# Performance work log

Hardware: AMD Instinct MI355X
Metric: run time of the kernel (lower is better)

Reference implementation:

```python
import jax, jax.numpy as jnp
import numpy as np

EPS = 1e-5
BS, NA, NC, NL, NPTS, ED, NG = 1, 900, 6, 4, 13, 256, 8
GD = ED // NG
IMG_W, IMG_H = 704.0, 256.0
FMAP_HW = [(64, 176), (32, 88), (16, 44), (8, 22)]


def _ln(x, g, b):
    m = x.mean(-1, keepdims=True)
    v = ((x - m) ** 2).mean(-1, keepdims=True)
    return (x - m) / jnp.sqrt(v + EPS) * g + b


def _grid_sample(img, grid):
    # img: [N,C,H,W]; grid: [N,P,Q,2] in [-1,1]; bilinear, zeros padding, align_corners=False
    N, C, H, W = img.shape
    gx = jnp.clip((grid[..., 0] + 1.0) * (W * 0.5) - 0.5, -1e4, 1e4)
    gy = jnp.clip((grid[..., 1] + 1.0) * (H * 0.5) - 0.5, -1e4, 1e4)
    x0 = jnp.floor(gx); y0 = jnp.floor(gy)
    wx1 = gx - x0; wy1 = gy - y0; wx0 = 1.0 - wx1; wy0 = 1.0 - wy1
    x0i = x0.astype(jnp.int32); y0i = y0.astype(jnp.int32)
    flat = img.reshape(N, C, H * W)

    def corner(xi, yi, wgt):
        valid = (xi >= 0) & (xi < W) & (yi >= 0) & (yi < H)
        idx = (jnp.clip(yi, 0, H - 1) * W + jnp.clip(xi, 0, W - 1))
        g = jax.vmap(lambda f, i: f[:, i])(flat, idx.reshape(N, -1))  # [N,C,P*Q]
        g = g.reshape(N, C, idx.shape[1], idx.shape[2])
        return g * (wgt * valid)[:, None]

    return (corner(x0i, y0i, wx0 * wy0) + corner(x0i + 1, y0i, wx1 * wy0)
            + corner(x0i, y0i + 1, wx0 * wy1) + corner(x0i + 1, y0i + 1, wx1 * wy1))


def setup_inputs() -> dict:
    key = jax.random.key(0)
    ks = jax.random.split(key, 20)
    d = {}
    d['instance_feature'] = jax.random.normal(ks[0], (BS, NA, ED), jnp.float32)
    xyz = jax.random.normal(ks[1], (BS, NA, 3), jnp.float32) * 1.5
    size = jax.random.normal(ks[2], (BS, NA, 3), jnp.float32) * 0.3
    theta = jax.random.uniform(ks[3], (BS, NA, 1), jnp.float32) * (2.0 * np.pi)
    vel = jax.random.normal(ks[4], (BS, NA, 3), jnp.float32) * 0.1
    d['anchor'] = jnp.concatenate([xyz, size, jnp.sin(theta), jnp.cos(theta), vel], -1)
    d['anchor_embed'] = jax.random.normal(ks[5], (BS, NA, ED), jnp.float32)
    for i, (h, w) in enumerate(FMAP_HW):
        d[f'fmap{i}'] = jax.random.normal(ks[6 + i], (BS, NC, ED, h, w), jnp.float32)
    base = jnp.array([[80., 0., 0., 352.], [0., 80., 0., 128.],
                      [0., 0., 0., 1.], [0., 0., 0., 1.]], jnp.float32)
    proj = jnp.tile(base, (BS, NC, 1, 1))
    proj = proj.at[:, :, :2, :].add(jax.random.normal(ks[10], (BS, NC, 2, 4), jnp.float32) * 2.0)
    d['projection_mat'] = proj
    d['image_wh'] = jnp.broadcast_to(jnp.array([IMG_W, IMG_H], jnp.float32), (BS, NC, 2))
    d['fix_scale'] = jnp.array([[0, 0, 0], [0.45, 0, 0], [-0.45, 0, 0], [0, 0.45, 0],
                                [0, -0.45, 0], [0, 0, 0.45], [0, 0, -0.45]], jnp.float32)

    def w(k, shape):
        return jax.random.normal(k, shape, jnp.float32) * 0.02

    d['lfc_w'] = w(ks[11], (ED, 6 * 3)); d['lfc_b'] = jnp.zeros((18,), jnp.float32)
    d['cam_w1'] = w(ks[12], (12, ED)); d['cam_b1'] = jnp.zeros((ED,), jnp.float32)
    d['cam_g1'] = jnp.ones((ED,), jnp.float32); d['cam_be1'] = jnp.zeros((ED,), jnp.float32)
    d['cam_w2'] = w(ks[13], (ED, ED)); d['cam_b2'] = jnp.zeros((ED,), jnp.float32)
    d['cam_g2'] = jnp.ones((ED,), jnp.float32); d['cam_be2'] = jnp.zeros((ED,), jnp.float32)
    d['wfc_w'] = w(ks[14], (ED, NG * NL * NPTS)); d['wfc_b'] = jnp.zeros((NG * NL * NPTS,), jnp.float32)
    d['op_w'] = w(ks[15], (ED, ED)); d['op_b'] = jnp.zeros((ED,), jnp.float32)
    return d


def reference(instance_feature, anchor, anchor_embed, fmap0, fmap1, fmap2, fmap3,
              projection_mat, image_wh, fix_scale, lfc_w, lfc_b,
              cam_w1, cam_b1, cam_g1, cam_be1, cam_w2, cam_b2, cam_g2, cam_be2,
              wfc_w, wfc_b, op_w, op_b):
    bs, na = instance_feature.shape[:2]
    # ---- keypoint generation ----
    size = jnp.exp(anchor[..., None, 3:6])                       # [bs,na,1,3]
    kp = fix_scale * size                                        # [bs,na,7,3]
    ls = jax.nn.sigmoid(instance_feature @ lfc_w + lfc_b).reshape(bs, na, -1, 3) - 0.5
    kp = jnp.concatenate([kp, ls * size], axis=-2)               # [bs,na,NPTS,3]
    sin, cos = anchor[..., 6:7], anchor[..., 7:8]                # [bs,na,1]
    kx, ky, kz = kp[..., 0], kp[..., 1], kp[..., 2]
    key_points = jnp.stack([cos * kx - sin * ky, sin * kx + cos * ky, kz], -1) \
                 + anchor[..., None, 0:3]                        # [bs,na,NPTS,3]
    # ---- per-cam/level/point group weights ----
    feat = instance_feature + anchor_embed
    cam_in = projection_mat[:, :, :3].reshape(bs, NC, 12)
    h = jax.nn.relu(cam_in @ cam_w1 + cam_b1); h = _ln(h, cam_g1, cam_be1)
    h = jax.nn.relu(h @ cam_w2 + cam_b2); cam_embed = _ln(h, cam_g2, cam_be2)
    f = feat[:, :, None] + cam_embed[:, None]                    # [bs,na,NC,ED]
    wts = (f @ wfc_w + wfc_b).reshape(bs, na, NC * NL * NPTS, NG)
    wts = jax.nn.softmax(wts, axis=-2).reshape(bs, na, NC, NL, NPTS, NG)
    # ---- multi-cam projection + bilinear sampling ----
    pts = jnp.concatenate([key_points, jnp.ones_like(key_points[..., :1])], -1)
    p2d = jnp.einsum('bcij,banj->bcani', projection_mat, pts)    # [bs,NC,na,NPTS,4]
    p2d = p2d[..., :2] / jnp.maximum(p2d[..., 2:3], 1e-5)
    p2d = p2d / image_wh[:, :, None, None]
    grid = (p2d * 2.0 - 1.0).reshape(bs * NC, na, NPTS, 2)
    feats = jnp.stack([_grid_sample(fm.reshape(bs * NC, ED, fm.shape[-2], fm.shape[-1]), grid)
                       for fm in (fmap0, fmap1, fmap2, fmap3)], axis=1)  # [bs*NC,NL,ED,na,NPTS]
    feats = feats.reshape(bs, NC, NL, ED, na, NPTS).transpose(0, 4, 1, 2, 5, 3)  # [bs,na,NC,NL,NPTS,ED]
    # ---- group-weighted fusion over cams & levels, then sum over points ----
    fg = feats.reshape(bs, na, NC, NL, NPTS, NG, GD)
    fused = jnp.einsum('bnclpg,bnclpgd->bnpgd', wts, fg).reshape(bs, na, NPTS, ED)
    fused = fused.sum(axis=2)                                    # [bs,na,ED]
    out = fused @ op_w + op_b
    return jnp.concatenate([out, instance_feature], axis=-1)     # [bs,na,2*ED]
```

## Files before the change

### kernel.cpp

```cpp
#include <hip/hip_runtime.h>
#include <stdint.h>

#define NA 900
#define NC 6
#define NL 4
#define NPTS 13
#define ED 256
#define NG 8
#define LNEPS 1e-5f
#define NSTAGE 718303
#define NSTAGE_BLOCKS 2806
#define NTRANS 5616
#define NCOPY 672
#define NSAMP 312

struct PIn { const void* p[24]; };

__device__ __forceinline__ float b2f(unsigned short u){
  union { uint32_t i; float f; } v; v.i = ((uint32_t)u)<<16; return v.f;
}
__device__ __forceinline__ unsigned short f2b(float f){
  union { float f; uint32_t i; } v; v.f = f;
  uint32_t r = v.i + 0x7FFFu + ((v.i>>16)&1u);
  return (unsigned short)(r>>16);
}
#define BLO(u) __uint_as_float((u)<<16)
#define BHI(u) __uint_as_float((u)&0xffff0000u)

__device__ __forceinline__ float ldx(const void* p, int i, bool bf){
  return bf ? b2f(((const unsigned short*)p)[i]) : ((const float*)p)[i];
}

__device__ __forceinline__ bool sniff_bf(const unsigned short* __restrict__ u16){
  int lane = threadIdx.x & 63;
  unsigned short u = u16[2*lane];
  int e = (u>>7)&0xFF;
  int sane = (e>=110 && e<=135) ? 1 : 0;
  #pragma unroll
  for (int m=32;m;m>>=1) sane += __shfl_xor(sane, m);
  return sane >= 48;
}

__device__ __forceinline__ void blockReduce2(float& a, float& b, float* lds){
  #pragma unroll
  for (int m=32;m;m>>=1){ a += __shfl_xor(a,m); b += __shfl_xor(b,m); }
  int w = threadIdx.x>>6;
  if ((threadIdx.x&63)==0){ lds[w]=a; lds[w+4]=b; }
  __syncthreads();
  a = lds[0]+lds[1]+lds[2]+lds[3];
  b = lds[4]+lds[5]+lds[6]+lds[7];
  __syncthreads();
}

__global__ __launch_bounds__(256) void k_prep(PIn in, float* __restrict__ stage,
                                              unsigned short* __restrict__ tf,
                                              unsigned short* __restrict__ wfcw_h,
                                              unsigned short* __restrict__ opw_h,
                                              float* __restrict__ Bc){
  const bool bf = sniff_bf((const unsigned short*)in.p[0]);
  const int tid = threadIdx.x;
  int b = blockIdx.x;

  __shared__ unsigned short T[64][68];
  __shared__ float h[ED];
  __shared__ float cE[ED];
  __shared__ float red8[8];
  __shared__ float part[4][64];

  if (b < NSTAGE_BLOCKS){
    const int cum[21] = {0,230400,240300,470700,470796,470808,470829,475437,475455,
                         478527,478783,479039,479295,544831,545087,545343,545599,
                         652095,652511,718047,718303};
    const int map[20] = {0,1,2,7,8,9,10,11,12,13,14,15,16,17,18,19,20,21,22,23};
    int idx = b*256 + tid;
    if (idx >= NSTAGE) return;
    int seg = 0, base = 0;
    #pragma unroll
    for (int s=1;s<20;s++) if (idx >= cum[s]){ seg = s; base = cum[s]; }
    const void* src = in.p[map[0]];
    #pragma unroll
    for (int s=1;s<20;s++) if (seg==s) src = in.p[map[s]];
    stage[idx] = ldx(src, idx - base, bf);
    return;
  }
  b -= NSTAGE_BLOCKS;
  if (b < NTRANS){
    const int xb[4]  = {176,44,11,3};
    const int HWs[4] = {11264,2816,704,176};
    const int TFO[4] = {0,17301504,21626880,22708224};
    int l, local;
    if      (b < 4224){ l=0; local=b;      }
    else if (b < 5280){ l=1; local=b-4224; }
    else if (b < 5544){ l=2; local=b-5280; }
    else              { l=3; local=b-5544; }
    int pt = local % xb[l]; int rest = local / xb[l];
    int ct = rest & 3; int c = rest >> 2;
    const int HW = HWs[l];
    const int px0 = pt*64;
    const void* src = in.p[3+l];
    #pragma unroll
    for (int p=0;p<2;p++){
      int lch = p*32 + (tid>>3);
      int gch = ct*64 + lch;
      int pxv = (tid&7)*8;
      size_t base = (size_t)(c*ED+gch)*HW + px0 + pxv;
      unsigned short v[8];
      if (px0 + pxv + 8 <= HW){
        if (bf){
          uint4 q = *reinterpret_cast<const uint4*>((const unsigned short*)src + base);
          v[0]=q.x&0xffff; v[1]=q.x>>16; v[2]=q.y&0xffff; v[3]=q.y>>16;
          v[4]=q.z&0xffff; v[5]=q.z>>16; v[6]=q.w&0xffff; v[7]=q.w>>16;
        } else {
          float4 f0 = *reinterpret_cast<const float4*>((const float*)src + base);
          float4 f1 = *reinterpret_cast<const float4*>((const float*)src + base + 4);
          v[0]=f2b(f0.x); v[1]=f2b(f0.y); v[2]=f2b(f0.z); v[3]=f2b(f0.w);
          v[4]=f2b(f1.x); v[5]=f2b(f1.y); v[6]=f2b(f1.z); v[7]=f2b(f1.w);
        }
      } else {
        #pragma unroll
        for (int i=0;i<8;i++){
          int px = px0+pxv+i;
          v[i] = (px<HW) ? (bf ? ((const unsigned short*)src)[base+i]
                               : f2b(((const float*)src)[base+i])) : (unsigned short)0;
        }
      }
      #pragma unroll
      for (int i=0;i<8;i++) T[pxv+i][lch] = v[i];
    }
    __syncthreads();
    unsigned short* dst = tf + TFO[l] + (size_t)c*HW*ED + ct*64;
    #pragma unroll
    for (int p=0;p<2;p++){
      int pxl = p*32 + (tid>>3);
      int px = px0 + pxl;
      if (px >= HW) continue;
      int ch8 = (tid&7)*8;
      ushort4 lo = *reinterpret_cast<ushort4*>(&T[pxl][ch8]);
      ushort4 hi = *reinterpret_cast<ushort4*>(&T[pxl][ch8+4]);
      union { ushort4 hh[2]; uint4 q; } u;
      u.hh[0]=lo; u.hh[1]=hi;
      *reinterpret_cast<uint4*>(dst + (size_t)px*ED + ch8) = u.q;
    }
    return;
  }
  b -= NTRANS;
  if (b < NCOPY){
    int idx = b*256 + tid;
    if (idx < 106496){
      wfcw_h[idx] = bf ? ((const unsigned short*)in.p[20])[idx]
                       : f2b(((const float*)in.p[20])[idx]);
    } else {
      int j = idx - 106496;
      opw_h[j] = bf ? ((const unsigned short*)in.p[22])[j]
                    : f2b(((const float*)in.p[22])[j]);
    }
    return;
  }
  b -= NCOPY;
  {
    const void* proj = in.p[7];
    const void* w1 = in.p[12]; const void* b1 = in.p[13];
    const void* g1 = in.p[14]; const void* be1 = in.p[15];
    const void* w2 = in.p[16]; const void* b2 = in.p[17];
    const void* g2 = in.p[18]; const void* be2 = in.p[19];
    const void* wfcw = in.p[20]; const void* wfcb = in.p[21];
    const int c = b/7, colt = b - (b/7)*7;
    float ci[12];
    #pragma unroll
    for (int i=0;i<12;i++) ci[i] = ldx(proj, c*16+i, bf);
    float acc = ldx(b1, tid, bf);
    #pragma unroll
    for (int k=0;k<12;k++) acc += ci[k]*ldx(w1, k*ED+tid, bf);
    float x = fmaxf(acc, 0.f);
    float s=x, q=x*x;
    blockReduce2(s,q,red8);
    float mean = s*(1.f/ED), var = q*(1.f/ED)-mean*mean;
    h[tid] = (x-mean)*rsqrtf(var+LNEPS)*ldx(g1,tid,bf) + ldx(be1,tid,bf);
    __syncthreads();
    acc = ldx(b2, tid, bf);
    #pragma unroll 8
    for (int k=0;k<ED;k++) acc += h[k]*ldx(w2, k*ED+tid, bf);
    x = fmaxf(acc,0.f);
    s=x; q=x*x;
    blockReduce2(s,q,red8);
    mean = s*(1.f/ED); var = q*(1.f/ED)-mean*mean;
    cE[tid] = (x-mean)*rsqrtf(var+LNEPS)*ldx(g2,tid,bf) + ldx(be2,tid,bf);
    __syncthreads();
    const int kc = tid>>6, colL = tid&63, col = colt*64+colL;
    float a = 0.f;
    if (col < 416){
      #pragma unroll 8
      for (int k=0;k<64;k++) a += cE[kc*64+k]*ldx(wfcw, (kc*64+k)*416+col, bf);
    }
    part[kc][colL] = a;
    __syncthreads();
    if (kc==0 && col<416)
      Bc[c*416+col] = part[0][colL]+part[1][colL]+part[2][colL]+part[3][colL] + ldx(wfcb,col,bf);
  }
}

__global__ __launch_bounds__(256) void k_anchor(
    const float* __restrict__ stage, const unsigned short* __restrict__ tf,
    const unsigned short* __restrict__ wfcw_h, const unsigned short* __restrict__ opw_h,
    const float* __restrict__ Bc, const void* __restrict__ rawinst,
    void* __restrict__ outv){
  const int n = blockIdx.x, tid = threadIdx.x;
  const bool bf = sniff_bf((const unsigned short*)rawinst);

  const float* s_inst = stage + 0;
  const float* s_anc  = stage + 230400;
  const float* s_ae   = stage + 240300;
  const float* s_proj = stage + 470700;
  const float* s_imwh = stage + 470796;
  const float* s_fixs = stage + 470808;
  const float* s_lw   = stage + 470829;
  const float* s_lb   = stage + 475437;
  const float* s_opb  = stage + 718047;

  __shared__ float ifs[ED];
  __shared__ float fe[ED];
  __shared__ float lg[NC*416];
  __shared__ uint4 cbi[NSAMP];
  __shared__ uint4 cwf[NSAMP];
  __shared__ unsigned short coff[NSAMP];
  __shared__ float red[8][ED+4];
  __shared__ float fu[ED];
  __shared__ float kp[13][3];
  __shared__ float sc[8];
  __shared__ float lsv[18];
  __shared__ int scnt;

  {
    if (tid==0) scnt = 0;
    float iv = s_inst[n*ED+tid];
    ifs[tid] = iv;
    fe[tid]  = iv + s_ae[n*ED+tid];
    if (tid < 3)       sc[tid] = s_anc[n*11+tid];
    else if (tid == 3) sc[3]   = s_anc[n*11+6];
    else if (tid == 4) sc[4]   = s_anc[n*11+7];
    else if (tid < 8)  sc[tid] = __expf(s_anc[n*11+tid-2]);
  }
  __syncthreads();
  if (tid < 144){
    int d = tid>>3, j = tid&7;
    float a = 0.f;
    #pragma unroll 8
    for (int k=j*32;k<j*32+32;k++) a += ifs[k]*s_lw[k*18+d];
    a += __shfl_xor(a,1); a += __shfl_xor(a,2); a += __shfl_xor(a,4);
    if (j==0){
      a += s_lb[d];
      lsv[d] = 1.f/(1.f+__expf(-a)) - 0.5f;
    }
  }
  __syncthreads();
  if (tid < 13){
    float kx,ky,kz;
    if (tid < 7){
      kx = s_fixs[tid*3+0]*sc[5];
      ky = s_fixs[tid*3+1]*sc[6];
      kz = s_fixs[tid*3+2]*sc[7];
    } else {
      int j = tid-7;
      kx = lsv[j*3+0]*sc[5]; ky = lsv[j*3+1]*sc[6]; kz = lsv[j*3+2]*sc[7];
    }
    kp[tid][0] = sc[4]*kx - sc[3]*ky + sc[0];
    kp[tid][1] = sc[3]*kx + sc[4]*ky + sc[1];
    kp[tid][2] = kz + sc[2];
  }
  {
    int col2 = (tid < 160) ? tid+256 : 415;
    float a0 = 0.f, a1 = 0.f;
    #pragma unroll 4
    for (int k=0;k<ED;k++){
      float fv = fe[k];
      a0 += fv*b2f(wfcw_h[k*416+tid]);
      a1 += fv*b2f(wfcw_h[k*416+col2]);
    }
    #pragma unroll
    for (int c=0;c<NC;c++){
      lg[c*416+tid] = a0 + Bc[c*416+tid];
      if (tid < 160) lg[c*416+tid+256] = a1 + Bc[c*416+tid+256];
    }
  }
  __syncthreads();
  #pragma unroll
  for (int pass=0;pass<2;pass++){
    int s = tid + pass*256;
    if (s < NSAMP){
      int c = s/52, rr = s - c*52;
      int l = rr/13, p = rr - l*13;
      float m[12];
      #pragma unroll
      for (int i=0;i<12;i++) m[i] = s_proj[c*16+i];
      float X=kp[p][0], Y=kp[p][1], Z=kp[p][2];
      float x = m[0]*X + m[1]*Y + m[2]*Z  + m[3];
      float y = m[4]*X + m[5]*Y + m[6]*Z  + m[7];
      float z = m[8]*X + m[9]*Y + m[10]*Z + m[11];
      float d = fmaxf(z, 1e-5f);
      float px = x/(d*s_imwh[c*2+0]), py = y/(d*s_imwh[c*2+1]);
      const int W = 176>>l, H = 64>>l;
      const int TFO[4] = {0,17301504,21626880,22708224};
      float gx = fminf(fmaxf(px*(float)W - 0.5f, -10000.f), 10000.f);
      float gy = fminf(fmaxf(py*(float)H - 0.5f, -10000.f), 10000.f);
      float xf = floorf(gx), yf = floorf(gy);
      int x0 = (int)xf, y0 = (int)yf;
      float wx1 = gx-xf, wy1 = gy-yf;
      float wx0 = 1.f-wx1, wy0 = 1.f-wy1;
      bool vx0 = (x0>=0)&&(x0<W),   vx1 = (x0+1>=0)&&(x0+1<W);
      bool vy0 = (y0>=0)&&(y0<H),   vy1 = (y0+1>=0)&&(y0+1<H);
      float w00 = (vx0&&vy0) ? wx0*wy0 : 0.f;
      float w10 = (vx1&&vy0) ? wx1*wy0 : 0.f;
      float w01 = (vx0&&vy1) ? wx0*wy1 : 0.f;
      float w11 = (vx1&&vy1) ? wx1*wy1 : 0.f;
      if (w00+w10+w01+w11 != 0.f){
        int cx0 = min(max(x0,0),W-1), cx1 = min(max(x0+1,0),W-1);
        int cy0 = min(max(y0,0),H-1), cy1 = min(max(y0+1,0),H-1);
        uint32_t cam = (uint32_t)TFO[l] + (uint32_t)(c*H*W)*ED;
        uint4 bi, wv;
        bi.x = cam + (uint32_t)(cy0*W+cx0)*ED;
        bi.y = cam + (uint32_t)(cy0*W+cx1)*ED;
        bi.z = cam + (uint32_t)(cy1*W+cx0)*ED;
        bi.w = cam + (uint32_t)(cy1*W+cx1)*ED;
        wv.x = __float_as_uint(w00); wv.y = __float_as_uint(w10);
        wv.z = __float_as_uint(w01); wv.w = __float_as_uint(w11);
        int slot = atomicAdd(&scnt, 1);
        cbi[slot] = bi;
        cwf[slot] = wv;
        coff[slot] = (unsigned short)(c*416 + rr*8);
      }
    }
  }
  {
    const int g = tid>>5, j = tid&31;
    float v[10]; float m = -1e30f;
    #pragma unroll
    for (int i=0;i<10;i++){
      int e = j + 32*i;
      float val = -1e30f;
      if (e < NSAMP){
        int c = e/52, rr = e - c*52;
        val = lg[c*416 + rr*8 + g];
        m = fmaxf(m, val);
      }
      v[i] = val;
    }
    #pragma unroll
    for (int mk=16;mk;mk>>=1) m = fmaxf(m, __shfl_xor(m, mk, 32));
    float sum = 0.f;
    #pragma unroll
    for (int i=0;i<10;i++){
      if (j + 32*i < NSAMP){ float ex = __expf(v[i]-m); v[i] = ex; sum += ex; }
    }
    #pragma unroll
    for (int mk=16;mk;mk>>=1) sum += __shfl_xor(sum, mk, 32);
    float inv = 1.f/sum;
    #pragma unroll
    for (int i=0;i<10;i++){
      int e = j + 32*i;
      if (e < NSAMP){
        int c = e/52, rr = e - c*52;
        lg[c*416 + rr*8 + g] = v[i]*inv;
      }
    }
  }
  __syncthreads();
  {
    const int m = scnt;
    const int strm = tid>>5, lane32 = tid&31;
    const int ch8 = lane32*8, gg = lane32>>2;
    float acc[8] = {0,0,0,0,0,0,0,0};
    int i = strm;
    for (; i + 8 < m; i += 16){
      uint4 biA = cbi[i],   wfA = cwf[i];
      uint4 biB = cbi[i+8], wfB = cwf[i+8];
      float wgA = lg[coff[i]+gg],  wgB = lg[coff[i+8]+gg];
      uint4 a00 = *reinterpret_cast<const uint4*>(tf + biA.x + ch8);
      uint4 a10 = *reinterpret_cast<const uint4*>(tf + biA.y + ch8);
      uint4 a01 = *reinterpret_cast<const uint4*>(tf + biA.z + ch8);
      uint4 a11 = *reinterpret_cast<const uint4*>(tf + biA.w + ch8);
      uint4 b00 = *reinterpret_cast<const uint4*>(tf + biB.x + ch8);
      uint4 b10 = *reinterpret_cast<const uint4*>(tf + biB.y + ch8);
      uint4 b01 = *reinterpret_cast<const uint4*>(tf + biB.z + ch8);
      uint4 b11 = *reinterpret_cast<const uint4*>(tf + biB.w + ch8);
      float pA00 = wgA*__uint_as_float(wfA.x), pA10 = wgA*__uint_as_float(wfA.y);
      float pA01 = wgA*__uint_as_float(wfA.z), pA11 = wgA*__uint_as_float(wfA.w);
      float pB00 = wgB*__uint_as_float(wfB.x), pB10 = wgB*__uint_as_float(wfB.y);
      float pB01 = wgB*__uint_as_float(wfB.z), pB11 = wgB*__uint_as_float(wfB.w);
      acc[0] += pA00*BLO(a00.x)+pA10*BLO(a10.x)+pA01*BLO(a01.x)+pA11*BLO(a11.x)
              + pB00*BLO(b00.x)+pB10*BLO(b10.x)+pB01*BLO(b01.x)+pB11*BLO(b11.x);
      acc[1] += pA00*BHI(a00.x)+pA10*BHI(a10.x)+pA01*BHI(a01.x)+pA11*BHI(a11.x)
              + pB00*BHI(b00.x)+pB10*BHI(b10.x)+pB01*BHI(b01.x)+pB11*BHI(b11.x);
      acc[2] += pA00*BLO(a00.y)+pA10*BLO(a10.y)+pA01*BLO(a01.y)+pA11*BLO(a11.y)
              + pB00*BLO(b00.y)+pB10*BLO(b10.y)+pB01*BLO(b01.y)+pB11*BLO(b11.y);
      acc[3] += pA00*BHI(a00.y)+pA10*BHI(a10.y)+pA01*BHI(a01.y)+pA11*BHI(a11.y)
              + pB00*BHI(b00.y)+pB10*BHI(b10.y)+pB01*BHI(b01.y)+pB11*BHI(b11.y);
      acc[4] += pA00*BLO(a00.z)+pA10*BLO(a10.z)+pA01*BLO(a01.z)+pA11*BLO(a11.z)
              + pB00*BLO(b00.z)+pB10*BLO(b10.z)+pB01*BLO(b01.z)+pB11*BLO(b11.z);
      acc[5] += pA00*BHI(a00.z)+pA10*BHI(a10.z)+pA01*BHI(a01.z)+pA11*BHI(a11.z)
              + pB00*BHI(b00.z)+pB10*BHI(b10.z)+pB01*BHI(b01.z)+pB11*BHI(b11.z);
      acc[6] += pA00*BLO(a00.w)+pA10*BLO(a10.w)+pA01*BLO(a01.w)+pA11*BLO(a11.w)
              + pB00*BLO(b00.w)+pB10*BLO(b10.w)+pB01*BLO(b01.w)+pB11*BLO(b11.w);
      acc[7] += pA00*BHI(a00.w)+pA10*BHI(a10.w)+pA01*BHI(a01.w)+pA11*BHI(a11.w)
              + pB00*BHI(b00.w)+pB10*BHI(b10.w)+pB01*BHI(b01.w)+pB11*BHI(b11.w);
    }
    for (; i < m; i += 8){
      uint4 bi = cbi[i], wf = cwf[i];
      float wg = lg[coff[i]+gg];
      uint4 q00 = *reinterpret_cast<const uint4*>(tf + bi.x + ch8);
      uint4 q10 = *reinterpret_cast<const uint4*>(tf + bi.y + ch8);
      uint4 q01 = *reinterpret_cast<const uint4*>(tf + bi.z + ch8);
      uint4 q11 = *reinterpret_cast<const uint4*>(tf + bi.w + ch8);
      float p00 = wg*__uint_as_float(wf.x), p10 = wg*__uint_as_float(wf.y);
      float p01 = wg*__uint_as_float(wf.z), p11 = wg*__uint_as_float(wf.w);
      acc[0] += p00*BLO(q00.x)+p10*BLO(q10.x)+p01*BLO(q01.x)+p11*BLO(q11.x);
      acc[1] += p00*BHI(q00.x)+p10*BHI(q10.x)+p01*BHI(q01.x)+p11*BHI(q11.x);
      acc[2] += p00*BLO(q00.y)+p10*BLO(q10.y)+p01*BLO(q01.y)+p11*BLO(q11.y);
      acc[3] += p00*BHI(q00.y)+p10*BHI(q10.y)+p01*BHI(q01.y)+p11*BHI(q11.y);
      acc[4] += p00*BLO(q00.z)+p10*BLO(q10.z)+p01*BLO(q01.z)+p11*BLO(q11.z);
      acc[5] += p00*BHI(q00.z)+p10*BHI(q10.z)+p01*BHI(q01.z)+p11*BHI(q11.z);
      acc[6] += p00*BLO(q00.w)+p10*BLO(q10.w)+p01*BLO(q01.w)+p11*BLO(q11.w);
      acc[7] += p00*BHI(q00.w)+p10*BHI(q10.w)+p01*BHI(q01.w)+p11*BHI(q11.w);
    }
    *reinterpret_cast<float4*>(&red[strm][ch8])   = make_float4(acc[0],acc[1],acc[2],acc[3]);
    *reinterpret_cast<float4*>(&red[strm][ch8+4]) = make_float4(acc[4],acc[5],acc[6],acc[7]);
  }
  __syncthreads();
  {
    float r = 0.f;
    #pragma unroll
    for (int i=0;i<8;i++) r += red[i][tid];
    fu[tid] = r;
  }
  __syncthreads();
  {
    float acc = s_opb[tid];
    #pragma unroll 4
    for (int k=0;k<ED;k++) acc += fu[k]*b2f(opw_h[k*ED+tid]);
    float pv = ifs[tid];
    if (bf){
      unsigned short* outh = (unsigned short*)outv;
      outh[n*512+tid]     = f2b(acc);
      outh[n*512+256+tid] = f2b(pv);
    } else {
      float* outf = (float*)outv;
      outf[n*512+tid]     = acc;
      outf[n*512+256+tid] = pv;
    }
  }
}

extern "C" void kernel_launch(void* const* d_in, const int* in_sizes, int n_in,
                              void* d_out, int out_size, void* d_ws, size_t ws_size,
                              hipStream_t stream){
  char* ws = (char*)d_ws;
  size_t off = 0;
  auto alloc = [&](size_t bytes)->char*{
    char* p = ws + off; off += (bytes + 63) & ~size_t(63); return p;
  };
  unsigned short* tf = (unsigned short*)alloc((size_t)22978560*2);
  float* stage  = (float*)alloc((size_t)NSTAGE*4);
  unsigned short* wfcw_h = (unsigned short*)alloc((size_t)106496*2);
  unsigned short* opw_h  = (unsigned short*)alloc((size_t)65536*2);
  float* Bc     = (float*)alloc((size_t)NC*416*4);

  PIn in;
  for (int i=0;i<24;i++) in.p[i] = d_in[i];

  k_prep<<<NSTAGE_BLOCKS + NTRANS + NCOPY + 42, 256, 0, stream>>>(in, stage, tf, wfcw_h, opw_h, Bc);
  k_anchor<<<NA, 256, 0, stream>>>(stage, tf, wfcw_h, opw_h, Bc, d_in[0], d_out);
}
```

Before: 255.8 us.

## Double k_anchor block to 512 threads and relayout softmax logits per group

Launches the per-anchor kernel with 512 threads instead of 256. The extra threads split the logit GEMV (one column per thread), the sample projection (a single pass), the gather streams (16 instead of 8) and the output projection (split-K over two halves). Logits are stored group-major with a padded stride, so the softmax reads them contiguously with full 64-lane wavefronts. This raises per-anchor parallelism and latency hiding in exchange for more threads per block, larger shared memory for the reduction buffer, and extra barriers.

```diff
diff --git a/kernel.cpp b/kernel.cpp
--- a/kernel.cpp
+++ b/kernel.cpp
@@ -13,6 +13,7 @@
 #define NTRANS 5616
 #define NCOPY 672
 #define NSAMP 312
+#define LGS 313
 
 struct PIn { const void* p[24]; };
 
@@ -199,7 +200,7 @@
   }
 }
 
-__global__ __launch_bounds__(256) void k_anchor(
+__global__ __launch_bounds__(512, 8) void k_anchor(
     const float* __restrict__ stage, const unsigned short* __restrict__ tf,
     const unsigned short* __restrict__ wfcw_h, const unsigned short* __restrict__ opw_h,
     const float* __restrict__ Bc, const void* __restrict__ rawinst,
@@ -219,26 +220,28 @@
 
   __shared__ float ifs[ED];
   __shared__ float fe[ED];
-  __shared__ float lg[NC*416];
+  __shared__ float lg2[8*LGS];
   __shared__ uint4 cbi[NSAMP];
   __shared__ uint4 cwf[NSAMP];
   __shared__ unsigned short coff[NSAMP];
-  __shared__ float red[8][ED+4];
+  __shared__ float red[16][ED+4];
   __shared__ float fu[ED];
   __shared__ float kp[13][3];
   __shared__ float sc[8];
   __shared__ float lsv[18];
   __shared__ int scnt;
 
-  {
-    if (tid==0) scnt = 0;
+  if (tid < 256){
     float iv = s_inst[n*ED+tid];
     ifs[tid] = iv;
     fe[tid]  = iv + s_ae[n*ED+tid];
-    if (tid < 3)       sc[tid] = s_anc[n*11+tid];
-    else if (tid == 3) sc[3]   = s_anc[n*11+6];
-    else if (tid == 4) sc[4]   = s_anc[n*11+7];
-    else if (tid < 8)  sc[tid] = __expf(s_anc[n*11+tid-2]);
+  } else {
+    int t = tid - 256;
+    if (t == 0)      scnt = 0;
+    if (t < 3)       sc[t] = s_anc[n*11+t];
+    else if (t == 3) sc[3] = s_anc[n*11+6];
+    else if (t == 4) sc[4] = s_anc[n*11+7];
+    else if (t < 8)  sc[t] = __expf(s_anc[n*11+t-2]);
   }
   __syncthreads();
   if (tid < 144){
@@ -267,100 +270,87 @@
     kp[tid][1] = sc[3]*kx + sc[4]*ky + sc[1];
     kp[tid][2] = kz + sc[2];
   }
+  if (tid < 416){
+    float a0 = 0.f;
+    #pragma unroll 8
+    for (int k=0;k<ED;k++) a0 += fe[k]*b2f(wfcw_h[k*416+tid]);
+    const int g = tid & 7, rr = tid >> 3;
+    #pragma unroll
+    for (int c=0;c<NC;c++)
+      lg2[g*LGS + c*52 + rr] = a0 + Bc[c*416+tid];
+  }
+  __syncthreads();
+  if (tid < NSAMP){
+    int s = tid;
+    int c = s/52, rr = s - c*52;
+    int l = rr/13, p = rr - l*13;
+    float m[12];
+    #pragma unroll
+    for (int i=0;i<12;i++) m[i] = s_proj[c*16+i];
+    float X=kp[p][0], Y=kp[p][1], Z=kp[p][2];
+    float x = m[0]*X + m[1]*Y + m[2]*Z  + m[3];
+    float y = m[4]*X + m[5]*Y + m[6]*Z  + m[7];
+    float z = m[8]*X + m[9]*Y + m[10]*Z + m[11];
+    float d = fmaxf(z, 1e-5f);
+    float px = x/(d*s_imwh[c*2+0]), py = y/(d*s_imwh[c*2+1]);
+    const int W = 176>>l, H = 64>>l;
+    const int TFO[4] = {0,17301504,21626880,22708224};
+    float gx = fminf(fmaxf(px*(float)W - 0.5f, -10000.f), 10000.f);
+    float gy = fminf(fmaxf(py*(float)H - 0.5f, -10000.f), 10000.f);
+    float xf = floorf(gx), yf = floorf(gy);
+    int x0 = (int)xf, y0 = (int)yf;
+    float wx1 = gx-xf, wy1 = gy-yf;
+    float wx0 = 1.f-wx1, wy0 = 1.f-wy1;
+    bool vx0 = (x0>=0)&&(x0<W),   vx1 = (x0+1>=0)&&(x0+1<W);
+    bool vy0 = (y0>=0)&&(y0<H),   vy1 = (y0+1>=0)&&(y0+1<H);
+    float w00 = (vx0&&vy0) ? wx0*wy0 : 0.f;
+    float w10 = (vx1&&vy0) ? wx1*wy0 : 0.f;
+    float w01 = (vx0&&vy1) ? wx0*wy1 : 0.f;
+    float w11 = (vx1&&vy1) ? wx1*wy1 : 0.f;
+    if (w00+w10+w01+w11 != 0.f){
+      int cx0 = min(max(x0,0),W-1), cx1 = min(max(x0+1,0),W-1);
+      int cy0 = min(max(y0,0),H-1), cy1 = min(max(y0+1,0),H-1);
+      uint32_t cam = (uint32_t)TFO[l] + (uint32_t)(c*H*W)*ED;
+      uint4 bi, wv;
+      bi.x = cam + (uint32_t)(cy0*W+cx0)*ED;
+      bi.y = cam + (uint32_t)(cy0*W+cx1)*ED;
+      bi.z = cam + (uint32_t)(cy1*W+cx0)*ED;
+      bi.w = cam + (uint32_t)(cy1*W+cx1)*ED;
+      wv.x = __float_as_uint(w00); wv.y = __float_as_uint(w10);
+      wv.z = __float_as_uint(w01); wv.w = __float_as_uint(w11);
+      int slot = atomicAdd(&scnt, 1);
+      cbi[slot] = bi;
+      cwf[slot] = wv;
+      coff[slot] = (unsigned short)s;
+    }
+  }
   {
-    int col2 = (tid < 160) ? tid+256 : 415;
-    float a0 = 0.f, a1 = 0.f;
-    #pragma unroll 4
-    for (int k=0;k<ED;k++){
-      float fv = fe[k];
-      a0 += fv*b2f(wfcw_h[k*416+tid]);
-      a1 += fv*b2f(wfcw_h[k*416+col2]);
-    }
-    #pragma unroll
-    for (int c=0;c<NC;c++){
-      lg[c*416+tid] = a0 + Bc[c*416+tid];
-      if (tid < 160) lg[c*416+tid+256] = a1 + Bc[c*416+tid+256];
-    }
-  }
-  __syncthreads();
-  #pragma unroll
-  for (int pass=0;pass<2;pass++){
-    int s = tid + pass*256;
-    if (s < NSAMP){
-      int c = s/52, rr = s - c*52;
-      int l = rr/13, p = rr - l*13;
-      float m[12];
-      #pragma unroll
-      for (int i=0;i<12;i++) m[i] = s_proj[c*16+i];
-      float X=kp[p][0], Y=kp[p][1], Z=kp[p][2];
-      float x = m[0]*X + m[1]*Y + m[2]*Z  + m[3];
-      float y = m[4]*X + m[5]*Y + m[6]*Z  + m[7];
-      float z = m[8]*X + m[9]*Y + m[10]*Z + m[11];
-      float d = fmaxf(z, 1e-5f);
-      float px = x/(d*s_imwh[c*2+0]), py = y/(d*s_imwh[c*2+1]);
-      const int W = 176>>l, H = 64>>l;
-      const int TFO[4] = {0,17301504,21626880,22708224};
-      float gx = fminf(fmaxf(px*(float)W - 0.5f, -10000.f), 10000.f);
-      float gy = fminf(fmaxf(py*(float)H - 0.5f, -10000.f), 10000.f);
-      float xf = floorf(gx), yf = floorf(gy);
-      int x0 = (int)xf, y0 = (int)yf;
-      float wx1 = gx-xf, wy1 = gy-yf;
-      float wx0 = 1.f-wx1, wy0 = 1.f-wy1;
-      bool vx0 = (x0>=0)&&(x0<W),   vx1 = (x0+1>=0)&&(x0+1<W);
-      bool vy0 = (y0>=0)&&(y0<H),   vy1 = (y0+1>=0)&&(y0+1<H);
-      float w00 = (vx0&&vy0) ? wx0*wy0 : 0.f;
-      float w10 = (vx1&&vy0) ? wx1*wy0 : 0.f;
-      float w01 = (vx0&&vy1) ? wx0*wy1 : 0.f;
-      float w11 = (vx1&&vy1) ? wx1*wy1 : 0.f;
-      if (w00+w10+w01+w11 != 0.f){
-        int cx0 = min(max(x0,0),W-1), cx1 = min(max(x0+1,0),W-1);
-        int cy0 = min(max(y0,0),H-1), cy1 = min(max(y0+1,0),H-1);
-        uint32_t cam = (uint32_t)TFO[l] + (uint32_t)(c*H*W)*ED;
-        uint4 bi, wv;
-        bi.x = cam + (uint32_t)(cy0*W+cx0)*ED;
-        bi.y = cam + (uint32_t)(cy0*W+cx1)*ED;
-        bi.z = cam + (uint32_t)(cy1*W+cx0)*ED;
-        bi.w = cam + (uint32_t)(cy1*W+cx1)*ED;
-        wv.x = __float_as_uint(w00); wv.y = __float_as_uint(w10);
-        wv.z = __float_as_uint(w01); wv.w = __float_as_uint(w11);
-        int slot = atomicAdd(&scnt, 1);
-        cbi[slot] = bi;
-        cwf[slot] = wv;
-        coff[slot] = (unsigned short)(c*416 + rr*8);
-      }
-    }
-  }
-  {
-    const int g = tid>>5, j = tid&31;
-    float v[10]; float m = -1e30f;
-    #pragma unroll
-    for (int i=0;i<10;i++){
-      int e = j + 32*i;
+    const int g = tid>>6, j = tid&63;
+    float v[5]; float mx = -1e30f;
+    #pragma unroll
+    for (int i=0;i<5;i++){
+      int e = j + 64*i;
       float val = -1e30f;
       if (e < NSAMP){
-        int c = e/52, rr = e - c*52;
-        val = lg[c*416 + rr*8 + g];
-        m = fmaxf(m, val);
+        val = lg2[g*LGS + e];
+        mx = fmaxf(mx, val);
       }
       v[i] = val;
     }
     #pragma unroll
-    for (int mk=16;mk;mk>>=1) m = fmaxf(m, __shfl_xor(m, mk, 32));
+    for (int mk=32;mk;mk>>=1) mx = fmaxf(mx, __shfl_xor(mx, mk));
     float sum = 0.f;
     #pragma unroll
-    for (int i=0;i<10;i++){
-      if (j + 32*i < NSAMP){ float ex = __expf(v[i]-m); v[i] = ex; sum += ex; }
-    }
-    #pragma unroll
-    for (int mk=16;mk;mk>>=1) sum += __shfl_xor(sum, mk, 32);
+    for (int i=0;i<5;i++){
+      if (j + 64*i < NSAMP){ float ex = __expf(v[i]-mx); v[i] = ex; sum += ex; }
+    }
+    #pragma unroll
+    for (int mk=32;mk;mk>>=1) sum += __shfl_xor(sum, mk);
     float inv = 1.f/sum;
     #pragma unroll
-    for (int i=0;i<10;i++){
-      int e = j + 32*i;
-      if (e < NSAMP){
-        int c = e/52, rr = e - c*52;
-        lg[c*416 + rr*8 + g] = v[i]*inv;
-      }
+    for (int i=0;i<5;i++){
+      int e = j + 64*i;
+      if (e < NSAMP) lg2[g*LGS + e] = v[i]*inv;
     }
   }
   __syncthreads();
@@ -370,10 +360,10 @@
     const int ch8 = lane32*8, gg = lane32>>2;
     float acc[8] = {0,0,0,0,0,0,0,0};
     int i = strm;
-    for (; i + 8 < m; i += 16){
-      uint4 biA = cbi[i],   wfA = cwf[i];
-      uint4 biB = cbi[i+8], wfB = cwf[i+8];
-      float wgA = lg[coff[i]+gg],  wgB = lg[coff[i+8]+gg];
+    for (; i + 16 < m; i += 32){
+      uint4 biA = cbi[i],    wfA = cwf[i];
+      uint4 biB = cbi[i+16], wfB = cwf[i+16];
+      float wgA = lg2[gg*LGS + coff[i]],  wgB = lg2[gg*LGS + coff[i+16]];
       uint4 a00 = *reinterpret_cast<const uint4*>(tf + biA.x + ch8);
       uint4 a10 = *reinterpret_cast<const uint4*>(tf + biA.y + ch8);
       uint4 a01 = *reinterpret_cast<const uint4*>(tf + biA.z + ch8);
@@ -403,9 +393,9 @@
       acc[7] += pA00*BHI(a00.w)+pA10*BHI(a10.w)+pA01*BHI(a01.w)+pA11*BHI(a11.w)
               + pB00*BHI(b00.w)+pB10*BHI(b10.w)+pB01*BHI(b01.w)+pB11*BHI(b11.w);
     }
-    for (; i < m; i += 8){
+    for (; i < m; i += 16){
       uint4 bi = cbi[i], wf = cwf[i];
-      float wg = lg[coff[i]+gg];
+      float wg = lg2[gg*LGS + coff[i]];
       uint4 q00 = *reinterpret_cast<const uint4*>(tf + bi.x + ch8);
       uint4 q10 = *reinterpret_cast<const uint4*>(tf + bi.y + ch8);
       uint4 q01 = *reinterpret_cast<const uint4*>(tf + bi.z + ch8);
@@ -425,27 +415,28 @@
     *reinterpret_cast<float4*>(&red[strm][ch8+4]) = make_float4(acc[4],acc[5],acc[6],acc[7]);
   }
   __syncthreads();
+  if (tid < 256){
+    float r = 0.f;
+    #pragma unroll
+    for (int i=0;i<16;i++) r += red[i][tid];
+    fu[tid] = r;
+  }
+  __syncthreads();
   {
-    float r = 0.f;
-    #pragma unroll
-    for (int i=0;i<8;i++) r += red[i][tid];
-    fu[tid] = r;
+    const int col = tid & 255, half = tid >> 8;
+    const int k0 = half*128;
+    float a = 0.f;
+    #pragma unroll 8
+    for (int k=k0;k<k0+128;k++) a += fu[k]*b2f(opw_h[k*ED+col]);
+    red[half][col] = a;
   }
   __syncthreads();
   {
-    float acc = s_opb[tid];
-    #pragma unroll 4
-    for (int k=0;k<ED;k++) acc += fu[k]*b2f(opw_h[k*ED+tid]);
-    float pv = ifs[tid];
-    if (bf){
-      unsigned short* outh = (unsigned short*)outv;
-      outh[n*512+tid]     = f2b(acc);
-      outh[n*512+256+tid] = f2b(pv);
-    } else {
-      float* outf = (float*)outv;
-      outf[n*512+tid]     = acc;
-      outf[n*512+256+tid] = pv;
-    }
+    float v;
+    if (tid < 256) v = s_opb[tid] + red[0][tid] + red[1][tid];
+    else           v = ifs[tid-256];
+    if (bf) ((unsigned short*)outv)[n*512+tid] = f2b(v);
+    else    ((float*)outv)[n*512+tid]          = v;
   }
 }
 
@@ -467,5 +458,5 @@
   for (int i=0;i<24;i++) in.p[i] = d_in[i];
 
   k_prep<<<NSTAGE_BLOCKS + NTRANS + NCOPY + 42, 256, 0, stream>>>(in, stage, tf, wfcw_h, opw_h, Bc);
-  k_anchor<<<NA, 256, 0, stream>>>(stage, tf, wfcw_h, opw_h, Bc, d_in[0], d_out);
-}
+  k_anchor<<<NA, 512, 0, stream>>>(stage, tf, wfcw_h, opw_h, Bc, d_in[0], d_out);
+}
```

After: 247.0 us. -3.4%, faster.
